# Optimization experiments

Hardware: AMD Instinct MI355X
Metric: run time of the kernel (lower is better)

## Reference

```python
import jax, jax.numpy as jnp
import numpy as np

MULT = 20.0 / 2 ** (5 - 2)  # level=2, num_levels=5, div_flow=20 -> 2.5
PATCH = 7
PAD = PATCH // 2


def up_flow_fn(flow, w):
    # ConvTranspose2d(2, 2, 4, stride=2, padding=1, groups=2, bias=False)
    wf = w[:, :, ::-1, ::-1]  # flip kernel -> equivalent dilated conv
    return jax.lax.conv_general_dilated(
        flow, wf, window_strides=(1, 1), padding=((2, 2), (2, 2)),
        lhs_dilation=(2, 2), dimension_numbers=('NCHW', 'OIHW', 'NCHW'),
        feature_group_count=2)


def warp(x, flow, mult):
    # ptlflow LiteFlowNet WarpingLayer: normalized grid + flow/div_flow, grid_sample
    # (border padding, align_corners=True) masked by zero-padded ones-sample >= 1.
    B, C, H, W = x.shape
    gx = jnp.linspace(-1.0, 1.0, W, dtype=x.dtype)[None, None, :]
    gy = jnp.linspace(-1.0, 1.0, H, dtype=x.dtype)[None, :, None]
    sx = gx + flow[:, 0] * (2.0 * mult / max(W - 1, 1))
    sy = gy + flow[:, 1] * (2.0 * mult / max(H - 1, 1))
    px = (sx + 1.0) * 0.5 * (W - 1)  # unnormalized coords, align_corners=True
    py = (sy + 1.0) * 0.5 * (H - 1)
    # --- border-padded bilinear sample of x ---
    pxc = jnp.clip(px, 0.0, W - 1.0)
    pyc = jnp.clip(py, 0.0, H - 1.0)
    x0 = jnp.floor(pxc); y0 = jnp.floor(pyc)
    tx = pxc - x0; ty = pyc - y0
    x0i = x0.astype(jnp.int32); y0i = y0.astype(jnp.int32)
    x1i = jnp.minimum(x0i + 1, W - 1); y1i = jnp.minimum(y0i + 1, H - 1)
    img = jnp.transpose(x, (0, 2, 3, 1))  # BHWC for gathers
    b = jnp.arange(B)[:, None, None]
    v00 = img[b, y0i, x0i]; v01 = img[b, y0i, x1i]
    v10 = img[b, y1i, x0i]; v11 = img[b, y1i, x1i]
    out = (v00 * ((1 - tx) * (1 - ty))[..., None] + v01 * (tx * (1 - ty))[..., None]
           + v10 * ((1 - tx) * ty)[..., None] + v11 * (tx * ty)[..., None])
    # --- zero-padded bilinear sample of ones -> validity mask ---
    fx0 = jnp.floor(px); fy0 = jnp.floor(py)
    mtx = px - fx0; mty = py - fy0
    m = jnp.zeros_like(px)
    for dy, dx, wgt in ((0, 0, (1 - mtx) * (1 - mty)), (0, 1, mtx * (1 - mty)),
                        (1, 0, (1 - mtx) * mty), (1, 1, mtx * mty)):
        xi = fx0 + dx; yi = fy0 + dy
        inb = (xi >= 0) & (xi <= W - 1) & (yi >= 0) & (yi <= H - 1)
        m = m + wgt * inb.astype(x.dtype)
    mask = (m >= 1.0).astype(x.dtype)[..., None]
    return jnp.transpose(out * mask, (0, 3, 1, 2))


def correlation(f1, f2):
    # SpatialCorrelationSampler(kernel_size=1, patch_size=7, stride=1, dilation_patch=1)
    # corr[b,d,i,j] = sum_c f1[b,c,i,j] * f2[b,c,i+di-3,j+dj-3] (zero pad), d = 7*di+dj
    B, C, H, W = f1.shape
    f2p = jnp.pad(f2, ((0, 0), (0, 0), (PAD, PAD), (PAD, PAD)))
    outs = [jnp.sum(f1 * f2p[:, :, di:di + H, dj:dj + W], axis=1)
            for di in range(PATCH) for dj in range(PATCH)]
    return jnp.stack(outs, axis=1)  # [B, 49, H, W]


def conv2d(x, w, b, pad):
    y = jax.lax.conv_general_dilated(
        x, w, window_strides=(1, 1), padding=((pad, pad), (pad, pad)),
        dimension_numbers=('NCHW', 'OIHW', 'NCHW'))
    return y + b[None, :, None, None]


def setup_inputs() -> dict:
    key = jax.random.key(0)
    ks = jax.random.split(key, 11)
    B, C, H, W = 4, 128, 192, 320
    feats = jax.random.normal(ks[0], (B, 2, C, H, W), jnp.float32)
    flow = jax.random.normal(ks[1], (B, 2, H // 2, W // 2), jnp.float32)
    up_w = jax.random.normal(ks[2], (2, 1, 4, 4), jnp.float32) * 0.25
    w1 = jax.random.normal(ks[3], (128, 49, 3, 3), jnp.float32) * 0.05
    b1 = jnp.zeros((128,), jnp.float32)
    w2 = jax.random.normal(ks[4], (64, 128, 3, 3), jnp.float32) * 0.03
    b2 = jnp.zeros((64,), jnp.float32)
    w3 = jax.random.normal(ks[5], (32, 64, 3, 3), jnp.float32) * 0.04
    b3 = jnp.zeros((32,), jnp.float32)
    w4 = jax.random.normal(ks[6], (2, 32, 5, 5), jnp.float32) * 0.03
    b4 = jnp.zeros((2,), jnp.float32)
    return {"feats": feats, "flow": flow, "up_w": up_w, "w1": w1, "b1": b1,
            "w2": w2, "b2": b2, "w3": w3, "b3": b3, "w4": w4, "b4": b4}


def reference(feats, flow, up_w, w1, b1, w2, b2, w3, b3, w4, b4):
    C = feats.shape[2]
    flow_up = up_flow_fn(flow, up_w)                    # [B,2,H,W]
    warped2 = warp(feats[:, 1], flow_up, MULT)          # warp feat2 by flow*mult
    corr = correlation(feats[:, 0], warped2)            # [B,49,H,W]
    corr = jax.nn.leaky_relu(corr, 0.1) / C
    h = jax.nn.leaky_relu(conv2d(corr, w1, b1, 1), 0.1)
    h = jax.nn.leaky_relu(conv2d(h, w2, b2, 1), 0.1)
    h = jax.nn.leaky_relu(conv2d(h, w3, b3, 1), 0.1)
    new_flow = conv2d(h, w4, b4, 2)                     # flow_kernel_size=5, pad=2
    return flow_up + new_flow
```

## Files before the change

### kernel.cpp

```cpp
#include <hip/hip_runtime.h>

typedef __attribute__((ext_vector_type(8))) short short8;
typedef __attribute__((ext_vector_type(4))) float f32x4;
typedef __attribute__((ext_vector_type(16))) float f32x16;
typedef unsigned int uint;

constexpr int B = 4, C = 128, H = 192, W = 320;
constexpr int HW_ = H * W;

__device__ __forceinline__ unsigned short f2bf(float x) {
    uint u = __float_as_uint(x);
    u += 0x7fffu + ((u >> 16) & 1u);
    return (unsigned short)(u >> 16);
}
__device__ __forceinline__ uint pack2bf(float a, float b) {
    return (uint)f2bf(a) | ((uint)f2bf(b) << 16);
}

__global__ __launch_bounds__(256) void upflow_kernel(
    const float* __restrict__ flow, const float* __restrict__ up_w,
    double* __restrict__ flow_up)
{
#pragma clang fp contract(off)
    int idx = blockIdx.x * 256 + threadIdx.x;
    if (idx >= B * 2 * HW_) return;
    int x = idx % W;
    int y = (idx / W) % H;
    int c = (idx / HW_) % 2;
    int b = idx / (2 * HW_);
    double acc = 0.0;
    #pragma unroll
    for (int ky = 0; ky < 4; ++ky) {
        int p = y + ky - 2;
        if (p < 0 || (p & 1) || (p >> 1) >= 96) continue;
        #pragma unroll
        for (int kx = 0; kx < 4; ++kx) {
            int q = x + kx - 2;
            if (q < 0 || (q & 1) || (q >> 1) >= 160) continue;
            double fv = (double)flow[((b * 2 + c) * 96 + (p >> 1)) * 160 + (q >> 1)];
            double wv = (double)up_w[c * 16 + (3 - ky) * 4 + (3 - kx)];
            double prod = fv * wv;
            acc = acc + prod;
        }
    }
    flow_up[idx] = acc;
}

__global__ __launch_bounds__(256) void warp_kernel(
    const float* __restrict__ feats, const double* __restrict__ flow_up,
    uint* __restrict__ wp)
{
#pragma clang fp contract(off)
    int g = blockIdx.x / 960;
    int idx = (blockIdx.x % 960) * 256 + threadIdx.x;
    int x = idx % W;
    int y = (idx / W) % H;
    int b = idx / HW_;

    double f0 = flow_up[(size_t)(b * 2 + 0) * HW_ + y * W + x];
    double f1 = flow_up[(size_t)(b * 2 + 1) * HW_ + y * W + x];

    double stepx = 2.0 / (double)(W - 1);
    double stepy = 2.0 / (double)(H - 1);
    double gx = (x == W - 1) ? 1.0 : ((double)x * stepx + (-1.0));
    double gy = (y == H - 1) ? 1.0 : ((double)y * stepy + (-1.0));
    double cxs = 2.0 * 2.5 / (double)(W - 1);
    double cys = 2.0 * 2.5 / (double)(H - 1);
    double sx = gx + f0 * cxs;
    double sy = gy + f1 * cys;
    double px = (sx + 1.0) * 0.5 * (double)(W - 1);
    double py = (sy + 1.0) * 0.5 * (double)(H - 1);

    double pxc = px < 0.0 ? 0.0 : (px > (double)(W - 1) ? (double)(W - 1) : px);
    double pyc = py < 0.0 ? 0.0 : (py > (double)(H - 1) ? (double)(H - 1) : py);
    double x0 = floor(pxc), y0 = floor(pyc);
    double tx = pxc - x0, ty = pyc - y0;
    int x0i = (int)x0, y0i = (int)y0;
    int y1i = min(y0i + 1, H - 1);

    double fx0 = floor(px), fy0 = floor(py);
    double mtx = px - fx0, mty = py - fy0;
    double w00 = (1.0 - mtx) * (1.0 - mty);
    double w01 = mtx * (1.0 - mty);
    double w10 = (1.0 - mtx) * mty;
    double w11 = mtx * mty;
    double m = 0.0;
    double xi, yi;
    xi = fx0;       yi = fy0;
    if (xi >= 0.0 && xi <= (double)(W - 1) && yi >= 0.0 && yi <= (double)(H - 1)) m = m + w00;
    xi = fx0 + 1.0; yi = fy0;
    if (xi >= 0.0 && xi <= (double)(W - 1) && yi >= 0.0 && yi <= (double)(H - 1)) m = m + w01;
    xi = fx0;       yi = fy0 + 1.0;
    if (xi >= 0.0 && xi <= (double)(W - 1) && yi >= 0.0 && yi <= (double)(H - 1)) m = m + w10;
    xi = fx0 + 1.0; yi = fy0 + 1.0;
    if (xi >= 0.0 && xi <= (double)(W - 1) && yi >= 0.0 && yi <= (double)(H - 1)) m = m + w11;
    float mask = (m >= 1.0) ? 1.0f : 0.0f;

    float a00 = (float)((1.0 - tx) * (1.0 - ty)) * mask;
    float a01 = (float)(tx * (1.0 - ty)) * mask;
    float a10 = (float)((1.0 - tx) * ty) * mask;
    float a11 = (float)(tx * ty) * mask;

    int base = min(x0i, W - 2);
    bool xe = (x0i == W - 1);
    int r0 = y0i * W + base;
    int r1 = y1i * W + base;

    const float* img = feats + (size_t)(b * 2 + 1) * C * HW_;
    uint* dst = wp + (size_t)b * 64 * HW_ + y * W + x;
    #pragma unroll 4
    for (int c2 = g * 32; c2 < g * 32 + 32; ++c2) {
        const float* p0 = img + (size_t)(2 * c2) * HW_;
        const float* p1 = p0 + HW_;
        float2 L0 = *(const float2*)&p0[r0];
        float2 L1 = *(const float2*)&p0[r1];
        float2 M0 = *(const float2*)&p1[r0];
        float2 M1 = *(const float2*)&p1[r1];
        float v00 = xe ? L0.y : L0.x;
        float v10 = xe ? L1.y : L1.x;
        float u00 = xe ? M0.y : M0.x;
        float u10 = xe ? M1.y : M1.x;
        float lo = a00 * v00 + a01 * L0.y + a10 * v10 + a11 * L1.y;
        float hi = a00 * u00 + a01 * M0.y + a10 * u10 + a11 * M1.y;
        dst[(size_t)c2 * HW_] = pack2bf(lo, hi);
    }
}

__global__ __launch_bounds__(256) void repack_w_kernel(
    const float* __restrict__ w1, const float* __restrict__ w2,
    const float* __restrict__ w3, const float* __restrict__ w4,
    unsigned short* __restrict__ wr)
{
    int idx = blockIdx.x * 256 + threadIdx.x;
    if (idx >= 178688) return;
    float v = 0.f;
    if (idx < 73728) {
        int tap = idx / 8192, r = idx % 8192, co = r / 64, ci = r % 64;
        if (ci < 49) v = w1[(co * 49 + ci) * 9 + tap];
    } else if (idx < 147456) {
        int i2 = idx - 73728;
        int tap = i2 / 8192, r = i2 % 8192, co = r / 128, ci = r % 128;
        v = w2[(co * 128 + ci) * 9 + tap];
    } else if (idx < 165888) {
        int i3 = idx - 147456;
        int tap = i3 / 2048, r = i3 % 2048, co = r / 64, ci = r % 64;
        v = w3[(co * 64 + ci) * 9 + tap];
    } else {
        int i4 = idx - 165888;
        int tap = i4 / 512, r = i4 % 512, co = r / 32, ci = r % 32;
        if (co < 2) v = w4[(co * 32 + ci) * 25 + tap];
    }
    wr[idx] = f2bf(v);
}

__global__ __launch_bounds__(256, 4) void corr_kernel(
    const float* __restrict__ feats, const uint* __restrict__ wp,
    uint* __restrict__ corrb)
{
    __shared__ unsigned short lds[(320 + 64) * 40];
    float* stage = (float*)lds;

    int t = blockIdx.x;
    int xt = t % 10, yg = (t / 10) % 96, b = t / 960;
    int x0 = xt * 32, y0 = yg * 2;
    int tid = threadIdx.x;
    int lane = tid & 63, wave = tid >> 6;
    int lanelo = lane & 15, laneq = (lane >> 4) & 3;
    int h = wave & 1, yr = wave >> 1;

    int baddr[10], di_t[10], c_t[10];
    #pragma unroll
    for (int tt = 0; tt < 10; ++tt) {
        int p = tt * 16 + lanelo;
        int di = p / 22, cc = p - di * 22;
        di_t[tt] = di; c_t[tt] = cc;
        int addr = ((yr + di) * 40 + h * 16 + cc + 1) * 40 + laneq * 8;
        baddr[tt] = (di > 6) ? 0 : addr;
    }
    int qaddr = (320 + yr * 32 + h * 16 + lanelo) * 40 + laneq * 8;

    f32x4 acc[10];
    #pragma unroll
    for (int tt = 0; tt < 10; ++tt) acc[tt] = f32x4{0.f, 0.f, 0.f, 0.f};

    const uint* wpb = wp + (size_t)b * 64 * HW_;
    const float* f1b = feats + (size_t)(b * 2) * C * HW_;

    for (int ck = 0; ck < 4; ++ck) {
        if (ck) __syncthreads();
        #pragma unroll
        for (int i = 0; i < 5; ++i) {
            int u = tid + i * 256;
            int q = u % 10, pp = (u / 10) & 15, r = u / 160;
            int gy = y0 - 3 + r, gx0 = x0 - 4 + 4 * q;
            uint4 v = {0, 0, 0, 0};
            if (gy >= 0 && gy < H && gx0 >= 0 && gx0 < W)
                v = *(const uint4*)&wpb[(size_t)(ck * 16 + pp) * HW_ + gy * W + gx0];
            int pxb = (r * 40 + 4 * q) * 40 + 2 * pp;
            *(uint*)&lds[pxb]       = v.x;
            *(uint*)&lds[pxb + 40]  = v.y;
            *(uint*)&lds[pxb + 80]  = v.z;
            *(uint*)&lds[pxb + 120] = v.w;
        }
        #pragma unroll
        for (int i = 0; i < 4; ++i) {
            int u = tid + i * 256;
            int px = u & 63, pp = u >> 6;
            int gx = x0 + (px & 31), gy = y0 + (px >> 5);
            const float* p0 = f1b + (size_t)(ck * 32 + 2 * pp) * HW_ + gy * W + gx;
            *(uint*)&lds[(320 + px) * 40 + 2 * pp] = pack2bf(p0[0], p0[HW_]);
        }
        __syncthreads();
        const short8 qf = *(const short8*)&lds[qaddr];
        #pragma unroll
        for (int tt = 0; tt < 10; ++tt) {
            const short8 kf = *(const short8*)&lds[baddr[tt]];
            acc[tt] = __builtin_amdgcn_mfma_f32_16x16x32_bf16(qf, kf, acc[tt], 0, 0, 0);
        }
    }
    __syncthreads();
    #pragma unroll
    for (int tt = 0; tt < 10; ++tt) {
        int di = di_t[tt];
        #pragma unroll
        for (int reg = 0; reg < 4; ++reg) {
            int i = laneq * 4 + reg;
            int dj = c_t[tt] - i;
            if (di <= 6 && dj >= 0 && dj < 7)
                stage[(di * 7 + dj) * 64 + yr * 32 + h * 16 + i] = acc[tt][reg];
        }
    }
    __syncthreads();
    uint* outp = corrb + (size_t)b * 32 * HW_;
    #pragma unroll
    for (int i = 0; i < 8; ++i) {
        int u = tid + i * 256;
        int px = u & 63, k2 = u >> 6;
        int gx = x0 + (px & 31), gy = y0 + (px >> 5);
        float v0 = (2 * k2 < 49) ? stage[(2 * k2) * 64 + px] : 0.f;
        float v1 = (2 * k2 + 1 < 49) ? stage[(2 * k2 + 1) * 64 + px] : 0.f;
        v0 = v0 > 0.f ? v0 : 0.1f * v0;
        v1 = v1 > 0.f ? v1 : 0.1f * v1;
        outp[(size_t)k2 * HW_ + gy * W + gx] = pack2bf(v0 * (1.f / 128.f), v1 * (1.f / 128.f));
    }
}

template<int CINP, int COUTP, int WCO, int WROWS, int MG, int NR, int MINW>
__global__ __launch_bounds__(256, MINW) void conv3x3_kernel(
    const uint* __restrict__ in, const unsigned short* __restrict__ wr,
    const float* __restrict__ bias, uint* __restrict__ outp)
{
    constexpr int TH = WROWS * NR;
    constexpr int RH = TH + 2;
    constexpr int RW = 40, S2 = 20;
    constexpr int CHUNKS = CINP / 32;
    __shared__ uint lds32[RH * RW * S2];

    int tid = threadIdx.x;
    int lane = tid & 63, wave = tid >> 6;
    int lane5 = lane & 31, kg = lane >> 5;
    int cow = (WCO == 1) ? 0 : (wave & 1);
    int rowg = (WCO == 1) ? wave : (wave >> 1);

    int bx = blockIdx.x;
    int xt = bx % 10;
    int yt = (bx / 10) % (H / TH);
    int b = bx / (10 * (H / TH));
    int tx0 = xt * 32, ty0 = yt * TH;
    int cob = cow * MG * 32;

    f32x16 acc[MG][NR];
    #pragma unroll
    for (int mg = 0; mg < MG; ++mg)
        #pragma unroll
        for (int nr = 0; nr < NR; ++nr)
            #pragma unroll
            for (int j = 0; j < 16; ++j) acc[mg][nr][j] = 0.f;

    const uint* inb = in + (size_t)b * (CINP / 2) * HW_;

    for (int ck = 0; ck < CHUNKS; ++ck) {
        if (ck) __syncthreads();
        constexpr int UNITS = RH * 10 * 16;
        for (int s = tid; s < UNITS; s += 256) {
            int q = s % 10;
            int pp = (s / 10) % 16;
            int r = s / 160;
            int gy = ty0 - 1 + r;
            int gx0 = tx0 - 4 + 4 * q;
            uint4 v = {0, 0, 0, 0};
            if (gy >= 0 && gy < H && gx0 >= 0 && gx0 < W)
                v = *(const uint4*)&inb[(size_t)(ck * 16 + pp) * HW_ + gy * W + gx0];
            int pbase = (r * RW + 4 * q) * S2 + pp;
            lds32[pbase]          = v.x;
            lds32[pbase + S2]     = v.y;
            lds32[pbase + 2 * S2] = v.z;
            lds32[pbase + 3 * S2] = v.w;
        }
        __syncthreads();

        for (int tap = 0; tap < 9; ++tap) {
            int ky = tap / 3, kx = tap - ky * 3;
            short8 A[MG][2];
            #pragma unroll
            for (int mg = 0; mg < MG; ++mg)
                #pragma unroll
                for (int ks = 0; ks < 2; ++ks)
                    A[mg][ks] = *(const short8*)&wr[
                        ((size_t)tap * COUTP + cob + mg * 32 + lane5) * CINP +
                        ck * 32 + ks * 16 + kg * 8];
            #pragma unroll
            for (int nr = 0; nr < NR; ++nr) {
                int rr = rowg * NR + nr + ky;
                int col = lane5 + kx + 3;
                #pragma unroll
                for (int ks = 0; ks < 2; ++ks) {
                    const short8 Bf = *(const short8*)&lds32[(rr * RW + col) * S2 + ks * 8 + kg * 4];
                    #pragma unroll
                    for (int mg = 0; mg < MG; ++mg)
                        acc[mg][nr] = __builtin_amdgcn_mfma_f32_32x32x16_bf16(
                            A[mg][ks], Bf, acc[mg][nr], 0, 0, 0);
                }
            }
        }
    }

    int xg = tx0 + lane5;
    #pragma unroll
    for (int mg = 0; mg < MG; ++mg)
        #pragma unroll
        for (int nr = 0; nr < NR; ++nr) {
            int ygl = ty0 + rowg * NR + nr;
            #pragma unroll
            for (int j = 0; j < 8; ++j) {
                int com = ((2 * j) & 3) + 8 * (j >> 1) + 4 * kg;
                int co = cob + mg * 32 + com;
                float v0 = acc[mg][nr][2 * j] + bias[co];
                float v1 = acc[mg][nr][2 * j + 1] + bias[co + 1];
                v0 = v0 > 0.f ? v0 : 0.1f * v0;
                v1 = v1 > 0.f ? v1 : 0.1f * v1;
                outp[((size_t)b * (COUTP / 2) + (co >> 1)) * HW_ + ygl * W + xg] =
                    pack2bf(v0, v1);
            }
        }
}

template<int CINP, int COUTP, int M_TILES, int N_TILES, int KS, int MINW>
__global__ __launch_bounds__(256, MINW) void conv_mfma_kernel(
    const uint* __restrict__ in, const unsigned short* __restrict__ wr,
    const float* __restrict__ bias, float* __restrict__ outp,
    const double* __restrict__ flow_up, int coutReal)
{
    constexpr int CHUNK = 32;
    constexpr int PADK = KS / 2;
    constexpr int PX_GROUPS = 4 / M_TILES;
    constexpr int TH = PX_GROUPS * (N_TILES / 2);
    constexpr int RH = TH + KS - 1;
    constexpr int RW = 40;
    constexpr int S2 = 20;
    constexpr int CHUNKS = CINP / CHUNK;
    __shared__ uint lds32[RH * RW * S2];

    int tid = threadIdx.x;
    int lanelo = tid & 15, laneq = (tid >> 4) & 3, wave = tid >> 6;
    int m_idx = wave % M_TILES, pgroup = wave / M_TILES;
    int pg_row0 = pgroup * (N_TILES / 2);

    int bx = blockIdx.x;
    int xt = bx % 10;
    int yt = (bx / 10) % (H / TH);
    int b = bx / (10 * (H / TH));
    int tx0 = xt * 32, ty0 = yt * TH;
    int cob = m_idx * 16;

    f32x4 acc[N_TILES];
    #pragma unroll
    for (int n = 0; n < N_TILES; ++n) acc[n] = f32x4{0.f, 0.f, 0.f, 0.f};

    const uint* inb = in + (size_t)b * (CINP / 2) * HW_;

    for (int ck = 0; ck < CHUNKS; ++ck) {
        constexpr int UNITS = RH * (CHUNK / 2) * 10;
        for (int s = tid; s < UNITS; s += 256) {
            int q = s % 10;
            int pp = (s / 10) % (CHUNK / 2);
            int r = s / (10 * (CHUNK / 2));
            int gy = ty0 - PADK + r;
            int gx0 = tx0 - 4 + q * 4;
            uint4 v = {0, 0, 0, 0};
            if (gy >= 0 && gy < H && gx0 >= 0 && gx0 < W)
                v = *(const uint4*)&inb[(size_t)(ck * (CHUNK / 2) + pp) * HW_ + gy * W + gx0];
            int pbase = (r * RW + q * 4) * S2 + pp;
            lds32[pbase] = v.x;
            lds32[pbase + S2] = v.y;
            lds32[pbase + 2 * S2] = v.z;
            lds32[pbase + 3 * S2] = v.w;
        }
        __syncthreads();

        short8 afr[KS * KS];
        #pragma unroll
        for (int tap = 0; tap < KS * KS; ++tap)
            afr[tap] = *(const short8*)&wr[
                ((size_t)tap * COUTP + cob + lanelo) * CINP + ck * CHUNK + laneq * 8];

        for (int tap = 0; tap < KS * KS; ++tap) {
            int ky = tap / KS, kx = tap - ky * KS;
            #pragma unroll
            for (int n = 0; n < N_TILES; ++n) {
                int rr = pg_row0 + (n >> 1) + ky;
                int pxi = (n & 1) * 16 + lanelo + (4 - PADK) + kx;
                const short8 bf = *(const short8*)&lds32[(rr * RW + pxi) * S2 + laneq * 4];
                acc[n] = __builtin_amdgcn_mfma_f32_16x16x32_bf16(afr[tap], bf, acc[n], 0, 0, 0);
            }
        }
        __syncthreads();
    }

    #pragma unroll
    for (int n = 0; n < N_TILES; ++n) {
        int x = tx0 + (n & 1) * 16 + lanelo;
        int y = ty0 + pg_row0 + (n >> 1);
        #pragma unroll
        for (int j = 0; j < 4; ++j) {
            int co = cob + laneq * 4 + j;
            if (co < coutReal) {
                float v = acc[n][j] + bias[co];
                v += (float)flow_up[((size_t)(b * 2) + co) * HW_ + y * W + x];
                outp[((size_t)b * coutReal + co) * HW_ + y * W + x] = v;
            }
        }
    }
}

extern "C" void kernel_launch(void* const* d_in, const int* in_sizes, int n_in,
                              void* d_out, int out_size, void* d_ws, size_t ws_size,
                              hipStream_t stream)
{
    const float* feats = (const float*)d_in[0];
    const float* flow  = (const float*)d_in[1];
    const float* up_w  = (const float*)d_in[2];
    const float* w1 = (const float*)d_in[3];
    const float* b1 = (const float*)d_in[4];
    const float* w2 = (const float*)d_in[5];
    const float* b2 = (const float*)d_in[6];
    const float* w3 = (const float*)d_in[7];
    const float* b3 = (const float*)d_in[8];
    const float* w4 = (const float*)d_in[9];
    const float* b4 = (const float*)d_in[10];
    float* out = (float*)d_out;

    char* ws = (char*)d_ws;
    double* flow_up = (double*)ws;
    uint* wp    = (uint*)(ws + 3932160);
    uint* h1    = (uint*)(ws + 3932160);
    uint* corrb = (uint*)(ws + 66846720);
    uint* h2    = corrb;
    uint* h3    = (uint*)(ws + 98304000);
    unsigned short* wr = (unsigned short*)(ws + 114032640);
    unsigned short* wr1 = wr;
    unsigned short* wr2 = wr + 73728;
    unsigned short* wr3 = wr + 147456;
    unsigned short* wr4 = wr + 165888;

    repack_w_kernel<<<699, 256, 0, stream>>>(w1, w2, w3, w4, wr);
    upflow_kernel<<<(B * 2 * HW_ + 255) / 256, 256, 0, stream>>>(flow, up_w, flow_up);
    warp_kernel<<<1920, 256, 0, stream>>>(feats, flow_up, wp);
    corr_kernel<<<3840, 256, 0, stream>>>(feats, wp, corrb);

    conv3x3_kernel<64, 128, 2, 2, 2, 2, 3>
        <<<1920, 256, 0, stream>>>(corrb, wr1, b1, h1);
    conv3x3_kernel<128, 64, 1, 4, 2, 2, 3>
        <<<960, 256, 0, stream>>>(h1, wr2, b2, h2);
    conv3x3_kernel<64, 32, 1, 4, 1, 2, 3>
        <<<960, 256, 0, stream>>>(h2, wr3, b3, h3);
    conv_mfma_kernel<32, 16, 1, 2, 5, 2>
        <<<1920, 256, 0, stream>>>(h3, wr4, b4, out, flow_up, 2);
}
```

Baseline: 781.2 us.

## Pad LDS strides and remap block order to spread tiles across XCDs

```diff
diff --git a/kernel.cpp b/kernel.cpp
--- a/kernel.cpp
+++ b/kernel.cpp
@@ -51,8 +51,10 @@
     uint* __restrict__ wp)
 {
 #pragma clang fp contract(off)
-    int g = blockIdx.x / 960;
-    int idx = (blockIdx.x % 960) * 256 + threadIdx.x;
+    int raw = blockIdx.x;
+    int eb  = (raw & 7) * 240 + (raw >> 3);
+    int g = eb / 960;
+    int idx = (eb % 960) * 256 + threadIdx.x;
     int x = idx % W;
     int y = (idx / W) % H;
     int b = idx / HW_;
@@ -157,10 +159,12 @@
     const float* __restrict__ feats, const uint* __restrict__ wp,
     uint* __restrict__ corrb)
 {
-    __shared__ unsigned short lds[(320 + 64) * 40];
+    constexpr int SP = 42;
+    __shared__ unsigned short lds[(320 + 64) * SP];
     float* stage = (float*)lds;
 
-    int t = blockIdx.x;
+    int raw = blockIdx.x;
+    int t = (raw & 7) * 480 + (raw >> 3);
     int xt = t % 10, yg = (t / 10) % 96, b = t / 960;
     int x0 = xt * 32, y0 = yg * 2;
     int tid = threadIdx.x;
@@ -174,10 +178,10 @@
         int p = tt * 16 + lanelo;
         int di = p / 22, cc = p - di * 22;
         di_t[tt] = di; c_t[tt] = cc;
-        int addr = ((yr + di) * 40 + h * 16 + cc + 1) * 40 + laneq * 8;
+        int addr = ((yr + di) * 40 + h * 16 + cc + 1) * SP + laneq * 8;
         baddr[tt] = (di > 6) ? 0 : addr;
     }
-    int qaddr = (320 + yr * 32 + h * 16 + lanelo) * 40 + laneq * 8;
+    int qaddr = (320 + yr * 32 + h * 16 + lanelo) * SP + laneq * 8;
 
     f32x4 acc[10];
     #pragma unroll
@@ -196,11 +200,11 @@
             uint4 v = {0, 0, 0, 0};
             if (gy >= 0 && gy < H && gx0 >= 0 && gx0 < W)
                 v = *(const uint4*)&wpb[(size_t)(ck * 16 + pp) * HW_ + gy * W + gx0];
-            int pxb = (r * 40 + 4 * q) * 40 + 2 * pp;
-            *(uint*)&lds[pxb]       = v.x;
-            *(uint*)&lds[pxb + 40]  = v.y;
-            *(uint*)&lds[pxb + 80]  = v.z;
-            *(uint*)&lds[pxb + 120] = v.w;
+            int pxb = (r * 40 + 4 * q) * SP + 2 * pp;
+            *(uint*)&lds[pxb]          = v.x;
+            *(uint*)&lds[pxb + SP]     = v.y;
+            *(uint*)&lds[pxb + 2 * SP] = v.z;
+            *(uint*)&lds[pxb + 3 * SP] = v.w;
         }
         #pragma unroll
         for (int i = 0; i < 4; ++i) {
@@ -208,7 +212,7 @@
             int px = u & 63, pp = u >> 6;
             int gx = x0 + (px & 31), gy = y0 + (px >> 5);
             const float* p0 = f1b + (size_t)(ck * 32 + 2 * pp) * HW_ + gy * W + gx;
-            *(uint*)&lds[(320 + px) * 40 + 2 * pp] = pack2bf(p0[0], p0[HW_]);
+            *(uint*)&lds[(320 + px) * SP + 2 * pp] = pack2bf(p0[0], p0[HW_]);
         }
         __syncthreads();
         const short8 qf = *(const short8*)&lds[qaddr];
@@ -227,7 +231,7 @@
             int i = laneq * 4 + reg;
             int dj = c_t[tt] - i;
             if (di <= 6 && dj >= 0 && dj < 7)
-                stage[(di * 7 + dj) * 64 + yr * 32 + h * 16 + i] = acc[tt][reg];
+                stage[(di * 7 + dj) * 65 + yr * 32 + h * 16 + i] = acc[tt][reg];
         }
     }
     __syncthreads();
@@ -237,8 +241,8 @@
         int u = tid + i * 256;
         int px = u & 63, k2 = u >> 6;
         int gx = x0 + (px & 31), gy = y0 + (px >> 5);
-        float v0 = (2 * k2 < 49) ? stage[(2 * k2) * 64 + px] : 0.f;
-        float v1 = (2 * k2 + 1 < 49) ? stage[(2 * k2 + 1) * 64 + px] : 0.f;
+        float v0 = (2 * k2 < 49) ? stage[(2 * k2) * 65 + px] : 0.f;
+        float v1 = (2 * k2 + 1 < 49) ? stage[(2 * k2 + 1) * 65 + px] : 0.f;
         v0 = v0 > 0.f ? v0 : 0.1f * v0;
         v1 = v1 > 0.f ? v1 : 0.1f * v1;
         outp[(size_t)k2 * HW_ + gy * W + gx] = pack2bf(v0 * (1.f / 128.f), v1 * (1.f / 128.f));
@@ -248,11 +252,11 @@
 template<int CINP, int COUTP, int WCO, int WROWS, int MG, int NR, int MINW>
 __global__ __launch_bounds__(256, MINW) void conv3x3_kernel(
     const uint* __restrict__ in, const unsigned short* __restrict__ wr,
-    const float* __restrict__ bias, uint* __restrict__ outp)
+    const float* __restrict__ bias, uint* __restrict__ outp, int cpx)
 {
     constexpr int TH = WROWS * NR;
     constexpr int RH = TH + 2;
-    constexpr int RW = 40, S2 = 20;
+    constexpr int RW = 40, S2 = 21;
     constexpr int CHUNKS = CINP / 32;
     __shared__ uint lds32[RH * RW * S2];
 
@@ -262,7 +266,8 @@
     int cow = (WCO == 1) ? 0 : (wave & 1);
     int rowg = (WCO == 1) ? wave : (wave >> 1);
 
-    int bx = blockIdx.x;
+    int raw = blockIdx.x;
+    int bx = (raw & 7) * cpx + (raw >> 3);
     int xt = bx % 10;
     int yt = (bx / 10) % (H / TH);
     int b = bx / (10 * (H / TH));
@@ -349,7 +354,7 @@
 __global__ __launch_bounds__(256, MINW) void conv_mfma_kernel(
     const uint* __restrict__ in, const unsigned short* __restrict__ wr,
     const float* __restrict__ bias, float* __restrict__ outp,
-    const double* __restrict__ flow_up, int coutReal)
+    const double* __restrict__ flow_up, int coutReal, int cpx)
 {
     constexpr int CHUNK = 32;
     constexpr int PADK = KS / 2;
@@ -357,7 +362,7 @@
     constexpr int TH = PX_GROUPS * (N_TILES / 2);
     constexpr int RH = TH + KS - 1;
     constexpr int RW = 40;
-    constexpr int S2 = 20;
+    constexpr int S2 = 21;
     constexpr int CHUNKS = CINP / CHUNK;
     __shared__ uint lds32[RH * RW * S2];
 
@@ -366,7 +371,8 @@
     int m_idx = wave % M_TILES, pgroup = wave / M_TILES;
     int pg_row0 = pgroup * (N_TILES / 2);
 
-    int bx = blockIdx.x;
+    int raw = blockIdx.x;
+    int bx = (raw & 7) * cpx + (raw >> 3);
     int xt = bx % 10;
     int yt = (bx / 10) % (H / TH);
     int b = bx / (10 * (H / TH));
@@ -469,11 +475,11 @@
     corr_kernel<<<3840, 256, 0, stream>>>(feats, wp, corrb);
 
     conv3x3_kernel<64, 128, 2, 2, 2, 2, 3>
-        <<<1920, 256, 0, stream>>>(corrb, wr1, b1, h1);
+        <<<1920, 256, 0, stream>>>(corrb, wr1, b1, h1, 240);
     conv3x3_kernel<128, 64, 1, 4, 2, 2, 3>
-        <<<960, 256, 0, stream>>>(h1, wr2, b2, h2);
+        <<<960, 256, 0, stream>>>(h1, wr2, b2, h2, 120);
     conv3x3_kernel<64, 32, 1, 4, 1, 2, 3>
-        <<<960, 256, 0, stream>>>(h2, wr3, b3, h3);
+        <<<960, 256, 0, stream>>>(h2, wr3, b3, h3, 120);
     conv_mfma_kernel<32, 16, 1, 2, 5, 2>
-        <<<1920, 256, 0, stream>>>(h3, wr4, b4, out, flow_up, 2);
-}
+        <<<1920, 256, 0, stream>>>(h3, wr4, b4, out, flow_up, 2, 240);
+}
```

Result: faster. 705.1 us (-9.7%).
